# Optimization experiments

Hardware: AMD Instinct MI355X
Metric: run time of the kernel (lower is better)

The kernel has to match this reference:

```python
import jax, jax.numpy as jnp
import numpy as np

# HT config: input_shape = output_shape = (8,8,8,8), rank = 8, d = 4 modes
B = 4096
M = 8      # per-mode input dim
N = 8      # per-mode output dim
R = 8      # HT rank
FEAT = M ** 4  # 4096


def setup_inputs() -> dict:
    key = jax.random.key(0)
    ks = jax.random.split(key, 8)
    x = jax.random.normal(ks[0], (B, FEAT), dtype=jnp.float32)
    # leaf factors: (in_p, out_p, rank); xavier-style scale over the input mode
    f_std = np.float32(np.sqrt(2.0 / (M + N * R)))
    F0 = jax.random.normal(ks[1], (M, N, R), dtype=jnp.float32) * f_std
    F1 = jax.random.normal(ks[2], (M, N, R), dtype=jnp.float32) * f_std
    F2 = jax.random.normal(ks[3], (M, N, R), dtype=jnp.float32) * f_std
    F3 = jax.random.normal(ks[4], (M, N, R), dtype=jnp.float32) * f_std
    # internal cores: (left_rank, right_rank, parent_rank)
    c_std = np.float32(np.sqrt(2.0 / (R + R * R)))
    CL = jax.random.normal(ks[5], (R, R, R), dtype=jnp.float32) * c_std
    CR = jax.random.normal(ks[6], (R, R, R), dtype=jnp.float32) * c_std
    bound = np.float32(1.0 / np.sqrt(FEAT))
    bias = jax.random.uniform(ks[7], (FEAT,), dtype=jnp.float32, minval=-bound, maxval=bound)
    return {"x": x, "F0": F0, "F1": F1, "F2": F2, "F3": F3,
            "CL": CL, "CR": CR, "bias": bias}


def reference(x, F0, F1, F2, F3, CL, CR, bias):
    b = x.shape[0]
    # (b, i, j, k, l): one axis per HT mode
    x4 = x.reshape(b, M, M, M, M)
    # Pre-contract each subtree's two leaves with its core (tiny tensors):
    # left transfer  W_L[i, j, a, c, p], right transfer W_R[k, l, d, e, p].
    # This is the same tensor-network contraction as the tn.Node graph,
    # just in an efficient associativity order.
    WL = jnp.einsum('iar,jcs,rsp->ijacp', F0, F1, CL)
    WR = jnp.einsum('kdr,les,rsp->kldep', F2, F3, CR)
    # contract left subtree against the input: (b, k, l, a, c, p)
    yL = jnp.einsum('bijkl,ijacp->bklacp', x4, WL)
    # contract right subtree; parent edges of the two subtrees are joined (p)
    y = jnp.einsum('bklacp,kldep->bacde', yL, WR)
    return y.reshape(b, FEAT) + bias
```

## Files before the change

kernel.cpp:

```cpp
#include <hip/hip_runtime.h>
#include <hip/hip_bf16.h>


typedef short bf16x8 __attribute__((ext_vector_type(8)));
typedef float f32x4  __attribute__((ext_vector_type(4)));

union Frag8 {
    bf16x8 v;
    unsigned int u4[4];
    uint2 u2[2];
};

static __device__ __forceinline__ unsigned int pkbf(float a, float b) {
    __hip_bfloat162 h = __float22bfloat162_rn(float2{a, b});
    return *reinterpret_cast<unsigned int*>(&h);
}

static __device__ __forceinline__ unsigned short f2bf(float f) {
    unsigned int u = __float_as_uint(f);
    u = (u + 0x7FFFu + ((u >> 16) & 1u)) >> 16;
    return (unsigned short)u;
}

__global__ void ht_precompute(const float* __restrict__ F0, const float* __restrict__ F1,
                              const float* __restrict__ F2, const float* __restrict__ F3,
                              const float* __restrict__ CL, const float* __restrict__ CR,
                              unsigned short* __restrict__ frags) {
    int idx = blockIdx.x * blockDim.x + threadIdx.x;
    int isW = idx >> 15;
    int r15 = idx & 32767;
    int p    = r15 >> 12;
    int f    = (r15 >> 9) & 7;
    int lane = (r15 >> 3) & 63;
    int j    = r15 & 7;
    int cb = f >> 1, ks = f & 1;
    int n = cb * 16 + (lane & 15);
    int k = ks * 32 + ((lane >> 4) & 3) * 8 + j;
    const float* Fa = isW ? F2 : F0;
    const float* Fb = isW ? F3 : F1;
    const float* C  = isW ? CR : CL;
    int i1 = k >> 3, i2 = k & 7, o1 = n >> 3, o2 = n & 7;
    float acc = 0.f;
    for (int r = 0; r < 8; ++r) {
        float fa = Fa[(i1 * 8 + o1) * 8 + r];
        for (int s = 0; s < 8; ++s)
            acc += fa * Fb[(i2 * 8 + o2) * 8 + s] * C[(r * 8 + s) * 8 + p];
    }
    frags[(size_t)isW * 32768 + ((p * 8 + f) << 9) + lane * 8 + j] = f2bf(acc);
}

#define T_PITCH 68

__global__ __launch_bounds__(256) void ht_main(const float* __restrict__ x,
                                               const unsigned short* __restrict__ frags,
                                               const float* __restrict__ bias,
                                               float* __restrict__ out) {
    __shared__ unsigned short Tl[4 * 64 * T_PITCH];
    const int tid  = threadIdx.x;
    const int lane = tid & 63;
    const int w    = __builtin_amdgcn_readfirstlane(tid >> 6);
    const int b    = blockIdx.x * 4 + w;
    unsigned short* Tw = Tl + w * (64 * T_PITCH);

    const int l15 = lane & 15;
    const int q   = lane >> 4;

    Frag8 xf[4][2];
    const float* xb = x + ((size_t)b << 12);
#pragma unroll
    for (int rb = 0; rb < 4; ++rb)
#pragma unroll
        for (int ks = 0; ks < 2; ++ks) {
            const float* src = xb + (ks * 32 + q * 8) * 64 + rb * 16 + l15;
#pragma unroll
            for (int j = 0; j < 8; j += 2)
                xf[rb][ks].u4[j >> 1] = pkbf(src[j * 64], src[(j + 1) * 64]);
        }

    f32x4 acc[4][4];
#pragma unroll
    for (int i = 0; i < 4; ++i)
#pragma unroll
        for (int j = 0; j < 4; ++j)
            acc[i][j] = f32x4{0.f, 0.f, 0.f, 0.f};

    const unsigned short* AF = frags;
    const unsigned short* WF = frags + 32768;

#pragma unroll 1
    for (int p = 0; p < 8; ++p) {
        Frag8 af[4][2];
#pragma unroll
        for (int cb = 0; cb < 4; ++cb)
#pragma unroll
            for (int ks = 0; ks < 2; ++ks)
                af[cb][ks].v = *(const bf16x8*)(AF + (((p * 8 + cb * 2 + ks) << 9) + lane * 8));
#pragma unroll
        for (int rb = 0; rb < 4; ++rb) {
#pragma unroll
            for (int cb = 0; cb < 4; ++cb) {
                f32x4 t = f32x4{0.f, 0.f, 0.f, 0.f};
                t = __builtin_amdgcn_mfma_f32_16x16x32_bf16(xf[rb][0].v, af[cb][0].v, t, 0, 0, 0);
                t = __builtin_amdgcn_mfma_f32_16x16x32_bf16(xf[rb][1].v, af[cb][1].v, t, 0, 0, 0);
                int ac = cb * 16 + l15;
                int kl = rb * 16 + q * 4;
                uint2 wv;
                wv.x = pkbf(t[0], t[1]);
                wv.y = pkbf(t[2], t[3]);
                *(uint2*)(&Tw[ac * T_PITCH + kl]) = wv;
            }
        }
        Frag8 wf[4][2];
#pragma unroll
        for (int cb = 0; cb < 4; ++cb)
#pragma unroll
            for (int ks = 0; ks < 2; ++ks)
                wf[cb][ks].v = *(const bf16x8*)(WF + (((p * 8 + cb * 2 + ks) << 9) + lane * 8));
        Frag8 tf[4][2];
#pragma unroll
        for (int rb = 0; rb < 4; ++rb)
#pragma unroll
            for (int ks = 0; ks < 2; ++ks) {
                int ac = rb * 16 + l15;
                int kl = ks * 32 + q * 8;
                tf[rb][ks].u2[0] = *(const uint2*)(&Tw[ac * T_PITCH + kl]);
                tf[rb][ks].u2[1] = *(const uint2*)(&Tw[ac * T_PITCH + kl + 4]);
            }
#pragma unroll
        for (int rb = 0; rb < 4; ++rb)
#pragma unroll
            for (int cb = 0; cb < 4; ++cb) {
                acc[rb][cb] = __builtin_amdgcn_mfma_f32_16x16x32_bf16(tf[rb][0].v, wf[cb][0].v, acc[rb][cb], 0, 0, 0);
                acc[rb][cb] = __builtin_amdgcn_mfma_f32_16x16x32_bf16(tf[rb][1].v, wf[cb][1].v, acc[rb][cb], 0, 0, 0);
            }
    }

    float* ob = out + ((size_t)b << 12);
#pragma unroll
    for (int rb = 0; rb < 4; ++rb)
#pragma unroll
        for (int cb = 0; cb < 4; ++cb) {
            int de  = cb * 16 + l15;
            int ac0 = rb * 16 + q * 4;
#pragma unroll
            for (int r = 0; r < 4; ++r) {
                int o = (ac0 + r) * 64 + de;
                ob[o] = acc[rb][cb][r] + bias[o];
            }
        }
}

extern "C" void kernel_launch(void* const* d_in, const int* in_sizes, int n_in,
                              void* d_out, int out_size, void* d_ws, size_t ws_size,
                              hipStream_t stream) {
    const float* x    = (const float*)d_in[0];
    const float* F0   = (const float*)d_in[1];
    const float* F1   = (const float*)d_in[2];
    const float* F2   = (const float*)d_in[3];
    const float* F3   = (const float*)d_in[4];
    const float* CL   = (const float*)d_in[5];
    const float* CR   = (const float*)d_in[6];
    const float* bias = (const float*)d_in[7];
    float* out = (float*)d_out;
    unsigned short* frags = (unsigned short*)d_ws;

    const int B = in_sizes[0] / 4096;

    ht_precompute<<<256, 256, 0, stream>>>(F0, F1, F2, F3, CL, CR, frags);
    ht_main<<<B / 4, 256, 0, stream>>>(x, frags, bias, out);
}
```

Baseline: 149.8 us.

## Switch to 32x32 MFMA with in-register intermediate via permlane32 swap

Replaces the 16x16x32 MFMA tiling with 32x32x16 MFMA tiles and reorganizes the precomputed fragment layout to match. The intermediate product is repacked in registers with permlane32_swap instead of going through an LDS transpose, so the per-p shared-memory round trip goes away. The second GEMM is transposed so the output is staged through an LDS buffer, which lets the stores be coalesced float2 writes with vectorized bias loads. It also sets launch_bounds to 2 blocks and unrolls the p loop by 2, which raises register pressure.

```diff
diff --git a/kernel.cpp b/kernel.cpp
--- a/kernel.cpp
+++ b/kernel.cpp
@@ -3,12 +3,11 @@
 
 
 typedef short bf16x8 __attribute__((ext_vector_type(8)));
-typedef float f32x4  __attribute__((ext_vector_type(4)));
+typedef float f32x16 __attribute__((ext_vector_type(16)));
 
 union Frag8 {
     bf16x8 v;
     unsigned int u4[4];
-    uint2 u2[2];
 };
 
 static __device__ __forceinline__ unsigned int pkbf(float a, float b) {
@@ -27,15 +26,15 @@
                               const float* __restrict__ CL, const float* __restrict__ CR,
                               unsigned short* __restrict__ frags) {
     int idx = blockIdx.x * blockDim.x + threadIdx.x;
-    int isW = idx >> 15;
-    int r15 = idx & 32767;
+    int isW  = idx >> 15;
+    int r15  = idx & 32767;
     int p    = r15 >> 12;
-    int f    = (r15 >> 9) & 7;
+    int t    = (r15 >> 11) & 1;
+    int kc   = (r15 >> 9) & 3;
     int lane = (r15 >> 3) & 63;
     int j    = r15 & 7;
-    int cb = f >> 1, ks = f & 1;
-    int n = cb * 16 + (lane & 15);
-    int k = ks * 32 + ((lane >> 4) & 3) * 8 + j;
+    int n = t * 32 + (lane & 31);
+    int k = kc * 16 + ((lane >> 5) & 1) * 8 + j;
     const float* Fa = isW ? F2 : F0;
     const float* Fb = isW ? F3 : F1;
     const float* C  = isW ? CR : CL;
@@ -46,108 +45,111 @@
         for (int s = 0; s < 8; ++s)
             acc += fa * Fb[(i2 * 8 + o2) * 8 + s] * C[(r * 8 + s) * 8 + p];
     }
-    frags[(size_t)isW * 32768 + ((p * 8 + f) << 9) + lane * 8 + j] = f2bf(acc);
+    frags[(size_t)isW * 32768 + ((((p * 2 + t) * 4 + kc) << 6) + lane) * 8 + j] = f2bf(acc);
 }
 
-#define T_PITCH 68
+#define Y_PITCH 66
 
-__global__ __launch_bounds__(256) void ht_main(const float* __restrict__ x,
-                                               const unsigned short* __restrict__ frags,
-                                               const float* __restrict__ bias,
-                                               float* __restrict__ out) {
-    __shared__ unsigned short Tl[4 * 64 * T_PITCH];
+__global__ __launch_bounds__(256, 2) void ht_main(const float* __restrict__ x,
+                                                  const unsigned short* __restrict__ frags,
+                                                  const float* __restrict__ bias,
+                                                  float* __restrict__ out) {
+    __shared__ float Ybuf[4][32 * Y_PITCH];
     const int tid  = threadIdx.x;
     const int lane = tid & 63;
     const int w    = __builtin_amdgcn_readfirstlane(tid >> 6);
     const int b    = blockIdx.x * 4 + w;
-    unsigned short* Tw = Tl + w * (64 * T_PITCH);
+    const int l31  = lane & 31;
+    const int hi   = lane >> 5;
 
-    const int l15 = lane & 15;
-    const int q   = lane >> 4;
-
-    Frag8 xf[4][2];
+    Frag8 xf[2][4];
     const float* xb = x + ((size_t)b << 12);
 #pragma unroll
-    for (int rb = 0; rb < 4; ++rb)
+    for (int rb = 0; rb < 2; ++rb)
 #pragma unroll
-        for (int ks = 0; ks < 2; ++ks) {
-            const float* src = xb + (ks * 32 + q * 8) * 64 + rb * 16 + l15;
+        for (int kc = 0; kc < 4; ++kc) {
+            const float* src = xb + (kc * 16 + hi * 8) * 64 + rb * 32 + l31;
 #pragma unroll
             for (int j = 0; j < 8; j += 2)
-                xf[rb][ks].u4[j >> 1] = pkbf(src[j * 64], src[(j + 1) * 64]);
+                xf[rb][kc].u4[j >> 1] = pkbf(src[j * 64], src[(j + 1) * 64]);
         }
 
-    f32x4 acc[4][4];
+    f32x16 acc[2][2];
 #pragma unroll
-    for (int i = 0; i < 4; ++i)
+    for (int i = 0; i < 2; ++i)
 #pragma unroll
-        for (int j = 0; j < 4; ++j)
-            acc[i][j] = f32x4{0.f, 0.f, 0.f, 0.f};
+        for (int j = 0; j < 2; ++j)
+#pragma unroll
+            for (int e = 0; e < 16; ++e)
+                acc[i][j][e] = 0.f;
 
     const unsigned short* AF = frags;
     const unsigned short* WF = frags + 32768;
 
-#pragma unroll 1
+#pragma unroll 2
     for (int p = 0; p < 8; ++p) {
-        Frag8 af[4][2];
+        Frag8 af[2][4], wf[2][4];
 #pragma unroll
-        for (int cb = 0; cb < 4; ++cb)
+        for (int t = 0; t < 2; ++t)
 #pragma unroll
-            for (int ks = 0; ks < 2; ++ks)
-                af[cb][ks].v = *(const bf16x8*)(AF + (((p * 8 + cb * 2 + ks) << 9) + lane * 8));
+            for (int kc = 0; kc < 4; ++kc) {
+                int off = (((p * 2 + t) * 4 + kc) << 9) + lane * 8;
+                af[t][kc].v = *(const bf16x8*)(AF + off);
+                wf[t][kc].v = *(const bf16x8*)(WF + off);
+            }
 #pragma unroll
-        for (int rb = 0; rb < 4; ++rb) {
+        for (int rb = 0; rb < 2; ++rb) {
 #pragma unroll
-            for (int cb = 0; cb < 4; ++cb) {
-                f32x4 t = f32x4{0.f, 0.f, 0.f, 0.f};
-                t = __builtin_amdgcn_mfma_f32_16x16x32_bf16(xf[rb][0].v, af[cb][0].v, t, 0, 0, 0);
-                t = __builtin_amdgcn_mfma_f32_16x16x32_bf16(xf[rb][1].v, af[cb][1].v, t, 0, 0, 0);
-                int ac = cb * 16 + l15;
-                int kl = rb * 16 + q * 4;
-                uint2 wv;
-                wv.x = pkbf(t[0], t[1]);
-                wv.y = pkbf(t[2], t[3]);
-                *(uint2*)(&Tw[ac * T_PITCH + kl]) = wv;
+            for (int cb = 0; cb < 2; ++cb) {
+                f32x16 t;
+#pragma unroll
+                for (int e = 0; e < 16; ++e) t[e] = 0.f;
+#pragma unroll
+                for (int kc = 0; kc < 4; ++kc)
+                    t = __builtin_amdgcn_mfma_f32_32x32x16_bf16(xf[rb][kc].v, af[cb][kc].v, t, 0, 0, 0);
+                unsigned int wd[8];
+#pragma unroll
+                for (int h = 0; h < 8; ++h) wd[h] = pkbf(t[2 * h], t[2 * h + 1]);
+                auto s02 = __builtin_amdgcn_permlane32_swap(wd[0], wd[2], false, false);
+                auto s13 = __builtin_amdgcn_permlane32_swap(wd[1], wd[3], false, false);
+                auto s46 = __builtin_amdgcn_permlane32_swap(wd[4], wd[6], false, false);
+                auto s57 = __builtin_amdgcn_permlane32_swap(wd[5], wd[7], false, false);
+                Frag8 tb0, tb1;
+                tb0.u4[0] = s02[0]; tb0.u4[1] = s13[0]; tb0.u4[2] = s02[1]; tb0.u4[3] = s13[1];
+                tb1.u4[0] = s46[0]; tb1.u4[1] = s57[0]; tb1.u4[2] = s46[1]; tb1.u4[3] = s57[1];
+                acc[0][cb] = __builtin_amdgcn_mfma_f32_32x32x16_bf16(wf[0][2 * rb].v,     tb0.v, acc[0][cb], 0, 0, 0);
+                acc[0][cb] = __builtin_amdgcn_mfma_f32_32x32x16_bf16(wf[0][2 * rb + 1].v, tb1.v, acc[0][cb], 0, 0, 0);
+                acc[1][cb] = __builtin_amdgcn_mfma_f32_32x32x16_bf16(wf[1][2 * rb].v,     tb0.v, acc[1][cb], 0, 0, 0);
+                acc[1][cb] = __builtin_amdgcn_mfma_f32_32x32x16_bf16(wf[1][2 * rb + 1].v, tb1.v, acc[1][cb], 0, 0, 0);
             }
         }
-        Frag8 wf[4][2];
+    }
+
+    float* Yw = &Ybuf[w][0];
+    float* ob = out + ((size_t)b << 12);
 #pragma unroll
-        for (int cb = 0; cb < 4; ++cb)
+    for (int cb = 0; cb < 2; ++cb) {
 #pragma unroll
-            for (int ks = 0; ks < 2; ++ks)
-                wf[cb][ks].v = *(const bf16x8*)(WF + (((p * 8 + cb * 2 + ks) << 9) + lane * 8));
-        Frag8 tf[4][2];
+        for (int mt = 0; mt < 2; ++mt)
 #pragma unroll
-        for (int rb = 0; rb < 4; ++rb)
-#pragma unroll
-            for (int ks = 0; ks < 2; ++ks) {
-                int ac = rb * 16 + l15;
-                int kl = ks * 32 + q * 8;
-                tf[rb][ks].u2[0] = *(const uint2*)(&Tw[ac * T_PITCH + kl]);
-                tf[rb][ks].u2[1] = *(const uint2*)(&Tw[ac * T_PITCH + kl + 4]);
+            for (int rp = 0; rp < 8; ++rp) {
+                int de = mt * 32 + 8 * (rp >> 1) + 2 * (rp & 1) + 4 * hi;
+                float2 v;
+                v.x = acc[mt][cb][2 * rp];
+                v.y = acc[mt][cb][2 * rp + 1];
+                *(float2*)(&Yw[l31 * Y_PITCH + de]) = v;
             }
 #pragma unroll
-        for (int rb = 0; rb < 4; ++rb)
-#pragma unroll
-            for (int cb = 0; cb < 4; ++cb) {
-                acc[rb][cb] = __builtin_amdgcn_mfma_f32_16x16x32_bf16(tf[rb][0].v, wf[cb][0].v, acc[rb][cb], 0, 0, 0);
-                acc[rb][cb] = __builtin_amdgcn_mfma_f32_16x16x32_bf16(tf[rb][1].v, wf[cb][1].v, acc[rb][cb], 0, 0, 0);
-            }
+        for (int i = 0; i < 16; ++i) {
+            int acl = 2 * i + hi;
+            float2 v = *(float2*)(&Yw[acl * Y_PITCH + 2 * l31]);
+            int o = (cb * 32 + acl) * 64 + 2 * l31;
+            float2 bv = *(const float2*)(bias + o);
+            v.x += bv.x;
+            v.y += bv.y;
+            *(float2*)(ob + o) = v;
+        }
     }
-
-    float* ob = out + ((size_t)b << 12);
-#pragma unroll
-    for (int rb = 0; rb < 4; ++rb)
-#pragma unroll
-        for (int cb = 0; cb < 4; ++cb) {
-            int de  = cb * 16 + l15;
-            int ac0 = rb * 16 + q * 4;
-#pragma unroll
-            for (int r = 0; r < 4; ++r) {
-                int o = (ac0 + r) * 64 + de;
-                ob[o] = acc[rb][cb][r] + bias[o];
-            }
-        }
 }
 
 extern "C" void kernel_launch(void* const* d_in, const int* in_sizes, int n_in,
```

After: 153.8 us. 1.03x slower.
